# Kernel tuning notes

Hardware: AMD Instinct MI355X
Metric: run time of the kernel (lower is better)

The kernel has to match this reference:

```python
import jax, jax.numpy as jnp
import numpy as np

D_MODEL = 1024
NUM_EXPERTS = 16
TOP_K = 2
TOP_C = 4  # min(M, max(4, 2*K))
RANK = 64  # max(4, d_model // 16) per choose_lowrank_r
TAU = 1.0


def setup_inputs() -> dict:
    key = jax.random.key(0)
    ks = jax.random.split(key, 7)
    B = 32768
    x = jax.random.normal(ks[0], (B, D_MODEL), dtype=jnp.float32)
    # shared encoder Linear(d, d) with bias
    We = jax.random.normal(ks[1], (D_MODEL, D_MODEL), dtype=jnp.float32) / np.sqrt(D_MODEL)
    be = jnp.zeros((D_MODEL,), dtype=jnp.float32)
    # gating Linear(d, M), no bias
    Wg = jax.random.normal(ks[2], (NUM_EXPERTS, D_MODEL), dtype=jnp.float32) / np.sqrt(D_MODEL)
    # per-expert LoRA weights: U: [M, r, d], V: [M, d, r], gamma: [M]
    U = jax.random.normal(ks[3], (NUM_EXPERTS, RANK, D_MODEL), dtype=jnp.float32) / np.sqrt(D_MODEL)
    V = jax.random.normal(ks[4], (NUM_EXPERTS, D_MODEL, RANK), dtype=jnp.float32) / np.sqrt(RANK)
    gamma = jnp.ones((NUM_EXPERTS,), dtype=jnp.float32)
    return {"x": x, "We": We, "be": be, "Wg": Wg, "U": U, "V": V, "gamma": gamma}


def reference(x, We, be, Wg, U, V, gamma):
    B = x.shape[0]
    encoded = x @ We.T + be                       # [B, d]
    logits = (encoded @ Wg.T) / TAU               # [B, M]
    # Top-C candidate selection, then Top-K among candidates
    topc_vals, topc_idx = jax.lax.top_k(logits, TOP_C)          # [B, C]
    topk_vals, pos_in_c = jax.lax.top_k(topc_vals, TOP_K)       # [B, K]
    topk_idx = jnp.take_along_axis(topc_idx, pos_in_c, axis=1)  # [B, K]
    # masked stable softmax over selected logits (matches _stable_masked_softmax)
    e = jnp.exp(topk_vals - jnp.max(topk_vals, axis=1, keepdims=True))
    w = e / (jnp.sum(e, axis=1, keepdims=True) + 1e-12)
    w = jnp.where(w > 1e-12, w, 0.0)  # keep_mask: drop negligible weights
    # scatter routing weights into dense [B, M] combine matrix
    w_full = jnp.zeros((B, NUM_EXPERTS), x.dtype).at[
        jnp.arange(B)[:, None], topk_idx].add(w)
    # expert residual delta: E(x) = x + gamma * V @ silu(U @ x)
    hidden = jax.nn.silu(jnp.einsum('bd,mrd->bmr', encoded, U))  # [B, M, r]
    delta = jnp.einsum('bmr,mdr,bm->bd', hidden, V, w_full * gamma[None, :])
    # y = encoded + sum_k w_k * (E_k(encoded) - encoded); sum_k w_k = 1
    return encoded + delta
```

## Files before the change

kernel.cpp:

```cpp
#include <hip/hip_runtime.h>
#include <stdint.h>

#define B_TOK 32768
#define DM 1024
#define NEXP 16
#define RK 64
#define NPAIR 256
#define TPT 64
#define HT 128
#define GRID_CMB 3072
#define GRID_HID 544
#define MAXTILE 1024

typedef unsigned short u16;
typedef __bf16 bf16x8 __attribute__((ext_vector_type(8)));
typedef float f32x4 __attribute__((ext_vector_type(4)));

__device__ __forceinline__ u16 f2bf(float f) {
  union { float f; uint32_t u; } v; v.f = f;
  return (u16)((v.u + 0x7fffu + ((v.u >> 16) & 1u)) >> 16);
}
__device__ __forceinline__ float bf2f(u16 u) {
  union { uint32_t i; float f; } v; v.i = ((uint32_t)u) << 16; return v.f;
}

__device__ __forceinline__ void gload_lds16(const void* g, void* l) {
  __builtin_amdgcn_global_load_lds(
      (const __attribute__((address_space(1))) void*)g,
      (__attribute__((address_space(3))) void*)l, 16, 0, 0);
}

__global__ void k_prep(const float* __restrict__ s0, u16* __restrict__ d0,
                       const float* __restrict__ s1, u16* __restrict__ d1,
                       const float* __restrict__ s2, u16* __restrict__ d2,
                       const float* __restrict__ Wg, const float* __restrict__ We,
                       double* __restrict__ Wpart) {
  const int b = blockIdx.x;
  if (b < 768) {
    const int seg = b >> 8;
    const int bid = b & 255;
    const float* src = (seg == 0) ? s0 : (seg == 1) ? s1 : s2;
    u16* dst = (seg == 0) ? d0 : (seg == 1) ? d1 : d2;
    int i = bid * 256 + threadIdx.x;
    #pragma unroll
    for (int v = 0; v < 4; ++v) {
      int idx = i + v * 65536;
      float4 f = reinterpret_cast<const float4*>(src)[idx];
      ushort4 o;
      o.x = f2bf(f.x); o.y = f2bf(f.y); o.z = f2bf(f.z); o.w = f2bf(f.w);
      reinterpret_cast<ushort4*>(dst)[idx] = o;
    }
  } else {
    const int pb = b - 768;
    const int kc = pb >> 6;
    const int rem = pb & 63;
    const int e = rem >> 2;
    const int bx = rem & 3;
    const int d = bx * 256 + threadIdx.x;
    const int kbase = kc * 256;
    double a0 = 0.0, a1 = 0.0, a2 = 0.0, a3 = 0.0;
    for (int k = 0; k < 256; k += 4) {
      int kk = kbase + k;
      a0 += (double)Wg[e * DM + kk]     * (double)We[(size_t)kk * DM + d];
      a1 += (double)Wg[e * DM + kk + 1] * (double)We[(size_t)(kk + 1) * DM + d];
      a2 += (double)Wg[e * DM + kk + 2] * (double)We[(size_t)(kk + 2) * DM + d];
      a3 += (double)Wg[e * DM + kk + 3] * (double)We[(size_t)(kk + 3) * DM + d];
    }
    Wpart[((size_t)kc * NEXP + e) * DM + d] = (a0 + a1) + (a2 + a3);
  }
}

__global__ void k_wgred(const double* __restrict__ Wpart, const float* __restrict__ Wg,
                        const float* __restrict__ be,
                        float* __restrict__ Wgeff, float* __restrict__ gbias) {
  const int e = blockIdx.y;
  const int d = blockIdx.x * 256 + threadIdx.x;
  double s = 0.0;
  #pragma unroll
  for (int kc = 0; kc < 4; ++kc)
    s += Wpart[((size_t)kc * NEXP + e) * DM + d];
  Wgeff[e * DM + d] = (float)s;
  if (blockIdx.x == 0 && threadIdx.x == 0) {
    double g = 0.0;
    for (int k = 0; k < DM; ++k) g += (double)be[k] * (double)Wg[e * DM + k];
    gbias[e] = (float)g;
  }
}

#define GT 64
#define GD 128

__global__ __launch_bounds__(256) void k_gating(
    const float* __restrict__ x, u16* __restrict__ x_bf,
    const float* __restrict__ Wgeff, const float* __restrict__ gbias,
    const float* __restrict__ gamma,
    int* __restrict__ tk_pid, float* __restrict__ tk_w0, float* __restrict__ tk_w1,
    int* __restrict__ counts_p, int* __restrict__ counts_e) {
  __shared__ float xs[GT][GD + 4];
  __shared__ float wsd[NEXP][GD + 4];
  __shared__ float lg[GT][NEXP + 2];
  __shared__ int bcnt[NPAIR];
  __shared__ int bexp[NEXP];
  const int tid = threadIdx.x;
  const int tok0 = blockIdx.x * GT;
  const int t0 = (tid >> 3) * 2;
  const int e0 = (tid & 7) * 2;
  bcnt[tid] = 0;
  if (tid < NEXP) bexp[tid] = 0;

  double acc00 = 0.0, acc01 = 0.0, acc10 = 0.0, acc11 = 0.0;

  for (int c = 0; c < DM; c += GD) {
    __syncthreads();
    #pragma unroll
    for (int v = 0; v < (GT * GD / 4) / 256; ++v) {
      int idx = tid + v * 256;
      int r = idx >> 5, cc = idx & 31;
      float4 v4 = *reinterpret_cast<const float4*>(x + (size_t)(tok0 + r) * DM + c + cc * 4);
      *reinterpret_cast<float4*>(&xs[r][cc * 4]) = v4;
      ushort4 o;
      o.x = f2bf(v4.x); o.y = f2bf(v4.y); o.z = f2bf(v4.z); o.w = f2bf(v4.w);
      *reinterpret_cast<ushort4*>(x_bf + (size_t)(tok0 + r) * DM + c + cc * 4) = o;
    }
    #pragma unroll
    for (int v = 0; v < (NEXP * GD / 4) / 256; ++v) {
      int idx = tid + v * 256;
      int r = idx >> 5, cc = idx & 31;
      *reinterpret_cast<float4*>(&wsd[r][cc * 4]) =
          *reinterpret_cast<const float4*>(Wgeff + (size_t)r * DM + c + cc * 4);
    }
    __syncthreads();
    #pragma unroll 8
    for (int d = 0; d < GD; d += 4) {
      float4 xa = *reinterpret_cast<const float4*>(&xs[t0][d]);
      float4 xb = *reinterpret_cast<const float4*>(&xs[t0 + 1][d]);
      float4 wa = *reinterpret_cast<const float4*>(&wsd[e0][d]);
      float4 wb = *reinterpret_cast<const float4*>(&wsd[e0 + 1][d]);
      acc00 += (double)xa.x * wa.x + (double)xa.y * wa.y + (double)xa.z * wa.z + (double)xa.w * wa.w;
      acc01 += (double)xa.x * wb.x + (double)xa.y * wb.y + (double)xa.z * wb.z + (double)xa.w * wb.w;
      acc10 += (double)xb.x * wa.x + (double)xb.y * wa.y + (double)xb.z * wa.z + (double)xb.w * wa.w;
      acc11 += (double)xb.x * wb.x + (double)xb.y * wb.y + (double)xb.z * wb.z + (double)xb.w * wb.w;
    }
  }

  lg[t0][e0]         = (float)(acc00 + (double)gbias[e0]);
  lg[t0][e0 + 1]     = (float)(acc01 + (double)gbias[e0 + 1]);
  lg[t0 + 1][e0]     = (float)(acc10 + (double)gbias[e0]);
  lg[t0 + 1][e0 + 1] = (float)(acc11 + (double)gbias[e0 + 1]);
  __syncthreads();

  if (tid < GT) {
    int tok = tok0 + tid;
    float v0 = lg[tid][0]; int i0 = 0;
    #pragma unroll
    for (int j = 1; j < NEXP; ++j)
      if (lg[tid][j] > v0) { v0 = lg[tid][j]; i0 = j; }
    float v1 = -3.4e38f; int i1 = 0;
    #pragma unroll
    for (int j = 0; j < NEXP; ++j) {
      if (j == i0) continue;
      if (lg[tid][j] > v1) { v1 = lg[tid][j]; i1 = j; }
    }
    float e1 = expf(v1 - v0);
    float denom = 1.0f + e1 + 1e-12f;
    float w0 = 1.0f / denom, w1 = e1 / denom;
    if (!(w0 > 1e-12f)) w0 = 0.0f;
    if (!(w1 > 1e-12f)) w1 = 0.0f;
    int pid = i0 * 16 + i1;
    tk_pid[tok] = pid;
    tk_w0[tok] = w0 * gamma[i0];
    tk_w1[tok] = w1 * gamma[i1];
    atomicAdd(&bcnt[pid], 1);
    atomicAdd(&bexp[i0], 1);
    atomicAdd(&bexp[i1], 1);
  }
  __syncthreads();
  if (bcnt[tid] > 0) atomicAdd(&counts_p[tid], bcnt[tid]);
  if (tid < NEXP && bexp[tid] > 0) atomicAdd(&counts_e[tid], bexp[tid]);
}

__global__ __launch_bounds__(NPAIR) void k_scan(
    const int* __restrict__ counts_p, const int* __restrict__ counts_e,
    int* __restrict__ offs_p, int* __restrict__ curs_p,
    int* __restrict__ offs_e, int* __restrict__ curs_e,
    int* __restrict__ tp_pair, int* __restrict__ tp_loc, int* __restrict__ n_tp,
    int* __restrict__ th_exp, int* __restrict__ th_loc, int* __restrict__ n_th) {
  __shared__ int sc[NPAIR], st[NPAIR];
  __shared__ int seb[NEXP + 1], thb[NEXP + 1];
  const int tid = threadIdx.x;
  const int c = counts_p[tid];
  const int nt = (c + TPT - 1) / TPT;
  sc[tid] = c; st[tid] = nt;
  __syncthreads();
  for (int s = 1; s < NPAIR; s <<= 1) {
    int vc = 0, vt = 0;
    if (tid >= s) { vc = sc[tid - s]; vt = st[tid - s]; }
    __syncthreads();
    sc[tid] += vc; st[tid] += vt;
    __syncthreads();
  }
  const int offc = sc[tid] - c;
  const int offt = st[tid] - nt;
  offs_p[tid] = offc;
  curs_p[tid] = offc;
  if (tid == NPAIR - 1) { offs_p[NPAIR] = sc[tid]; n_tp[0] = st[tid]; }
  for (int q = 0; q < nt; ++q) { tp_pair[offt + q] = tid; tp_loc[offt + q] = q * TPT; }

  if (tid == 0) {
    int s = 0, s2 = 0;
    for (int e = 0; e < NEXP; ++e) {
      seb[e] = s; thb[e] = s2;
      int ce = counts_e[e];
      s += ce; s2 += (ce + HT - 1) / HT;
    }
    seb[NEXP] = s; thb[NEXP] = s2;
    n_th[0] = s2;
  }
  __syncthreads();
  if (tid <= NEXP) offs_e[tid] = seb[tid];
  if (tid < NEXP) {
    curs_e[tid] = seb[tid];
    int ce = counts_e[tid];
    int ntt = (ce + HT - 1) / HT;
    for (int q = 0; q < ntt; ++q) { th_exp[thb[tid] + q] = tid; th_loc[thb[tid] + q] = q * HT; }
  }
}

__global__ __launch_bounds__(256) void k_scatter(
    const int* __restrict__ tk_pid, const float* __restrict__ tk_w0,
    const float* __restrict__ tk_w1,
    int* __restrict__ curs_p, int* __restrict__ curs_e,
    int* __restrict__ a_tok, int* __restrict__ a_h0,
    int* __restrict__ a_h1,
    int* __restrict__ e_tok, float* __restrict__ e_w) {
  __shared__ int hp[NPAIR];
  __shared__ int he[NEXP];
  __shared__ int bp[NPAIR];
  __shared__ int beB[NEXP];
  const int tid = threadIdx.x;
  const int tok = blockIdx.x * 256 + tid;
  hp[tid] = 0;
  if (tid < NEXP) he[tid] = 0;
  __syncthreads();

  const int pid = tk_pid[tok];
  const int i0 = pid >> 4, i1 = pid & 15;
  const int rp = atomicAdd(&hp[pid], 1);
  const int r0 = atomicAdd(&he[i0], 1);
  const int r1 = atomicAdd(&he[i1], 1);
  __syncthreads();

  if (hp[tid] > 0) bp[tid] = atomicAdd(&curs_p[tid], hp[tid]);
  if (tid < NEXP && he[tid] > 0) beB[tid] = atomicAdd(&curs_e[tid], he[tid]);
  __syncthreads();

  const int posp = bp[pid] + rp;
  const int pos0 = beB[i0] + r0;
  const int pos1 = beB[i1] + r1;
  a_tok[posp] = tok;
  a_h0[posp] = pos0;
  a_h1[posp] = pos1;
  e_tok[pos0] = tok; e_w[pos0] = tk_w0[tok];
  e_tok[pos1] = tok; e_w[pos1] = tk_w1[tok];
}

__global__ __launch_bounds__(256) void k_encoder(
    const u16* __restrict__ A, const u16* __restrict__ Bm,
    const float* __restrict__ bias, u16* __restrict__ Cb) {
  __shared__ __align__(16) u16 As0[128 * 64];
  __shared__ __align__(16) u16 Bs0[128 * 64];
  __shared__ __align__(16) u16 As1[128 * 64];
  __shared__ __align__(16) u16 Bs1[128 * 64];
  const int nwg = gridDim.x * gridDim.y;
  const int orig = blockIdx.y * gridDim.x + blockIdx.x;
  const int qq = nwg >> 3;
  const int swz = (orig & 7) * qq + (orig >> 3);
  const int m0 = (swz / gridDim.x) * 128, n0 = (swz % gridDim.x) * 128;
  const int tid = threadIdx.x;
  const int lane = tid & 63, wave = tid >> 6;
  const int wr = wave >> 1, wc = wave & 1;
  const int lrow = lane & 15, lhi = lane >> 4;

  f32x4 acc[4][4];
  #pragma unroll
  for (int i = 0; i < 4; ++i)
    #pragma unroll
    for (int j = 0; j < 4; ++j) acc[i][j] = (f32x4){0.f, 0.f, 0.f, 0.f};

  const u16* gA0; const u16* gA1; const u16* gA2; const u16* gA3;
  const u16* gB0; const u16* gB1; const u16* gB2; const u16* gB3;
  int dOf0, dOf1, dOf2, dOf3;
  {
    int slot, row, c, sc;
    slot = tid;         row = slot >> 3; c = slot & 7; sc = (c ^ (row & 7)) * 8;
    gA0 = A + (size_t)(m0 + row) * DM + sc; gB0 = Bm + (size_t)(n0 + row) * DM + sc; dOf0 = slot * 8;
    slot = tid + 256;   row = slot >> 3; c = slot & 7; sc = (c ^ (row & 7)) * 8;
    gA1 = A + (size_t)(m0 + row) * DM + sc; gB1 = Bm + (size_t)(n0 + row) * DM + sc; dOf1 = slot * 8;
    slot = tid + 512;   row = slot >> 3; c = slot & 7; sc = (c ^ (row & 7)) * 8;
    gA2 = A + (size_t)(m0 + row) * DM + sc; gB2 = Bm + (size_t)(n0 + row) * DM + sc; dOf2 = slot * 8;
    slot = tid + 768;   row = slot >> 3; c = slot & 7; sc = (c ^ (row & 7)) * 8;
    gA3 = A + (size_t)(m0 + row) * DM + sc; gB3 = Bm + (size_t)(n0 + row) * DM + sc; dOf3 = slot * 8;
  }

  const int rk0 = ((0 + lhi) ^ (lrow & 7)) * 8;
  const int rk1 = ((4 + lhi) ^ (lrow & 7)) * 8;

  auto STAGE = [&](u16* Ad, u16* Bd, int k0) {
    gload_lds16(gA0 + k0, Ad + dOf0);
    gload_lds16(gA1 + k0, Ad + dOf1);
    gload_lds16(gA2 + k0, Ad + dOf2);
    gload_lds16(gA3 + k0, Ad + dOf3);
    gload_lds16(gB0 + k0, Bd + dOf0);
    gload_lds16(gB1 + k0, Bd + dOf1);
    gload_lds16(gB2 + k0, Bd + dOf2);
    gload_lds16(gB3 + k0, Bd + dOf3);
  };
  auto COMPUTE = [&](const u16* Ar, const u16* Br) {
    #pragma unroll
    for (int kk = 0; kk < 2; ++kk) {
      const int rk = kk ? rk1 : rk0;
      bf16x8 a[4], b[4];
      #pragma unroll
      for (int mi = 0; mi < 4; ++mi)
        a[mi] = *reinterpret_cast<const bf16x8*>(&Ar[(wr * 64 + mi * 16 + lrow) * 64 + rk]);
      #pragma unroll
      for (int nj = 0; nj < 4; ++nj)
        b[nj] = *reinterpret_cast<const bf16x8*>(&Br[(wc * 64 + nj * 16 + lrow) * 64 + rk]);
      #pragma unroll
      for (int mi = 0; mi < 4; ++mi)
        #pragma unroll
        for (int nj = 0; nj < 4; ++nj)
          acc[mi][nj] = __builtin_amdgcn_mfma_f32_16x16x32_bf16(a[mi], b[nj], acc[mi][nj], 0, 0, 0);
    }
  };

  STAGE(As0, Bs0, 0);
  #pragma unroll
  for (int i = 0; i < 8; ++i) {
    STAGE(As1, Bs1, i * 128 + 64);
    asm volatile("s_waitcnt vmcnt(8)" ::: "memory");
    __builtin_amdgcn_s_barrier();
    COMPUTE(As0, Bs0);
    __builtin_amdgcn_s_barrier();
    if (i < 7) {
      STAGE(As0, Bs0, i * 128 + 128);
      asm volatile("s_waitcnt vmcnt(8)" ::: "memory");
    } else {
      asm volatile("s_waitcnt vmcnt(0)" ::: "memory");
    }
    __builtin_amdgcn_s_barrier();
    COMPUTE(As1, Bs1);
    __builtin_amdgcn_s_barrier();
  }

  const int orow = lhi * 4, ocol = lrow;
  #pragma unroll
  for (int mi = 0; mi < 4; ++mi) {
    #pragma unroll
    for (int nj = 0; nj < 4; ++nj) {
      int gcol = n0 + wc * 64 + nj * 16 + ocol;
      float bv = bias[gcol];
      #pragma unroll
      for (int r = 0; r < 4; ++r) {
        int grow = m0 + wr * 64 + mi * 16 + orow + r;
        Cb[(size_t)grow * DM + gcol] = f2bf(acc[mi][nj][r] + bv);
      }
    }
  }
}

__global__ __launch_bounds__(256) void k_hidden(
    const u16* __restrict__ Enc, const u16* __restrict__ Ub,
    const int* __restrict__ offs_e, const int* __restrict__ th_exp,
    const int* __restrict__ th_loc, const int* __restrict__ n_th,
    const int* __restrict__ e_tok, const float* __restrict__ e_w,
    u16* __restrict__ Hws) {
  const int bswz = (blockIdx.x & 7) * (GRID_HID >> 3) + (blockIdx.x >> 3);
  if (bswz >= n_th[0]) return;
  const int e = th_exp[bswz];
  const int loc0 = th_loc[bswz];
  const int base = offs_e[e];
  const int cnt = offs_e[e + 1] - base;
  const int tid = threadIdx.x;
  const int lane = tid & 63, wave = tid >> 6;
  const int lrow = lane & 15;
  const int lkb = (lane >> 4) * 16;

  __shared__ float s_ew[HT];
  __shared__ __align__(16) u16 Us[64 * 512];
  if (tid < HT) {
    int i = loc0 + tid;
    s_ew[tid] = (i < cnt) ? e_w[base + i] : 0.0f;
  }

  const u16* aP[2];
  #pragma unroll
  for (int mi = 0; mi < 2; ++mi) {
    int ridx = loc0 + wave * 32 + mi * 16 + lrow;
    int v = ridx < cnt;
    int tok = e_tok[base + (v ? ridx : 0)];
    aP[mi] = Enc + (size_t)tok * DM + (lane >> 4) * 8;
  }

  f32x4 acc[2][4];
  #pragma unroll
  for (int i = 0; i < 2; ++i)
    #pragma unroll
    for (int j = 0; j < 4; ++j) acc[i][j] = (f32x4){0.f, 0.f, 0.f, 0.f};

  const char* Ue = (const char*)(Ub + (size_t)e * RK * DM);

  for (int half = 0; half < 2; ++half) {
    __syncthreads();
    #pragma unroll
    for (int it = 0; it < 16; ++it) {
      int D = (tid + it * 256) * 16;
      int row = D >> 10, bo = D & 1023;
      int sbo = bo ^ ((row & 7) << 4);
      gload_lds16(Ue + (size_t)row * 2048 + half * 1024 + sbo, ((char*)Us) + D);
    }
    __syncthreads();
    #pragma unroll 4
    for (int step = 0; step < 16; ++step) {
      const int k0 = half * 512 + step * 32;
      bf16x8 b[4];
      #pragma unroll
      for (int nj = 0; nj < 4; ++nj) {
        int n = nj * 16 + lrow;
        int bofs = n * 1024 + ((step * 64 + lkb) ^ ((n & 7) << 4));
        b[nj] = *reinterpret_cast<const bf16x8*>(((const char*)Us) + bofs);
      }
      bf16x8 a0 = *reinterpret_cast<const bf16x8*>(aP[0] + k0);
      bf16x8 a1 = *reinterpret_cast<const bf16x8*>(aP[1] + k0);
      #pragma unroll
      for (int nj = 0; nj < 4; ++nj) {
        acc[0][nj] = __builtin_amdgcn_mfma_f32_16x16x32_bf16(a0, b[nj], acc[0][nj], 0, 0, 0);
        acc[1][nj] = __builtin_amdgcn_mfma_f32_16x16x32_bf16(a1, b[nj], acc[1][nj], 0, 0, 0);
      }
    }
  }

  #pragma unroll
  for (int mi = 0; mi < 2; ++mi)
    #pragma unroll
    for (int nj = 0; nj < 4; ++nj)
      #pragma unroll
      for (int rr = 0; rr < 4; ++rr) {
        int rloc = wave * 32 + mi * 16 + (lane >> 4) * 4 + rr;
        if (loc0 + rloc < cnt) {
          float z = acc[mi][nj][rr];
          float h = z / (1.0f + expf(-z)) * s_ew[rloc];
          Hws[(size_t)(base + loc0 + rloc) * RK + nj * 16 + (lane & 15)] = f2bf(h);
        }
      }
}

__global__ __launch_bounds__(256) void k_combine(
    const u16* __restrict__ Enc, const u16* __restrict__ Vb,
    const u16* __restrict__ Hws, const int* __restrict__ offs_p,
    const int* __restrict__ tp_pair, const int* __restrict__ tp_loc,
    const int* __restrict__ n_tp, const int* __restrict__ a_tok,
    const int* __restrict__ a_h0, const int* __restrict__ a_h1,
    float* __restrict__ Out) {
  const int bswz = (blockIdx.x & 7) * (GRID_CMB >> 3) + (blockIdx.x >> 3);
  const int t = bswz >> 2;
  const int p = bswz & 3;
  if (t >= n_tp[0]) return;
  const int pid = tp_pair[t];
  const int pe0 = pid >> 4, pe1 = pid & 15;
  const int base = offs_p[pid];
  const int cnt = offs_p[pid + 1] - base;
  const int loc0 = tp_loc[t];
  const int tid = threadIdx.x;
  const int lane = tid & 63, wave = tid >> 6;

  __shared__ int s_tok[TPT];
  __shared__ int s_h0[TPT];
  __shared__ int s_h1[TPT];
  __shared__ int s_val[TPT];
  if (tid < TPT) {
    int idx = loc0 + tid;
    int v = idx < cnt;
    int pp = base + (v ? idx : 0);
    s_val[tid] = v;
    s_tok[tid] = a_tok[pp];
    s_h0[tid] = a_h0[pp];
    s_h1[tid] = a_h1[pp];
  }
  __syncthreads();

  const int lrow = lane & 15, lk = (lane >> 4) * 8;
  const int col0 = p * 256 + wave * 64;

  bf16x8 hb[4][4];
  #pragma unroll
  for (int kk = 0; kk < 4; ++kk)
    #pragma unroll
    for (int tf = 0; tf < 4; ++tf) {
      int tok = tf * 16 + lrow;
      int hidx = (kk < 2) ? s_h0[tok] : s_h1[tok];
      hb[kk][tf] = *reinterpret_cast<const bf16x8*>(
          Hws + (size_t)hidx * RK + (kk & 1) * 32 + lk);
    }

  ushort4 encv[4][4];
  #pragma unroll
  for (int mi = 0; mi < 4; ++mi)
    #pragma unroll
    for (int tf = 0; tf < 4; ++tf) {
      int tok = tf * 16 + (lane & 15);
      int d = col0 + mi * 16 + (lane >> 4) * 4;
      encv[mi][tf] = *reinterpret_cast<const ushort4*>(Enc + (size_t)s_tok[tok] * DM + d);
    }

  const u16* V0 = Vb + (size_t)pe0 * DM * RK;
  const u16* V1 = Vb + (size_t)pe1 * DM * RK;

  f32x4 acc2[4][4];
  #pragma unroll
  for (int i = 0; i < 4; ++i)
    #pragma unroll
    for (int j = 0; j < 4; ++j) acc2[i][j] = (f32x4){0.f, 0.f, 0.f, 0.f};

  #pragma unroll
  for (int kk = 0; kk < 4; ++kk) {
    const u16* Vsel = (kk < 2) ? V0 : V1;
    const int kof = (kk & 1) * 32 + lk;
    #pragma unroll
    for (int mi = 0; mi < 4; ++mi) {
      int d = col0 + mi * 16 + lrow;
      bf16x8 va = *reinterpret_cast<const bf16x8*>(Vsel + (size_t)d * RK + kof);
      #pragma unroll
      for (int tf = 0; tf < 4; ++tf)
        acc2[mi][tf] = __builtin_amdgcn_mfma_f32_16x16x32_bf16(va, hb[kk][tf], acc2[mi][tf], 0, 0, 0);
    }
  }

  #pragma unroll
  for (int mi = 0; mi < 4; ++mi)
    #pragma unroll
    for (int tf = 0; tf < 4; ++tf) {
      int tok = tf * 16 + (lane & 15);
      if (!s_val[tok]) continue;
      int d = col0 + mi * 16 + (lane >> 4) * 4;
      size_t ro = (size_t)s_tok[tok] * DM + d;
      ushort4 ev = encv[mi][tf];
      float4 o;
      o.x = acc2[mi][tf][0] + bf2f(ev.x);
      o.y = acc2[mi][tf][1] + bf2f(ev.y);
      o.z = acc2[mi][tf][2] + bf2f(ev.z);
      o.w = acc2[mi][tf][3] + bf2f(ev.w);
      *reinterpret_cast<float4*>(Out + ro) = o;
    }
}

extern "C" void kernel_launch(void* const* d_in, const int* in_sizes, int n_in,
                              void* d_out, int out_size, void* d_ws, size_t ws_size,
                              hipStream_t stream) {
  const float* x = (const float*)d_in[0];
  const float* We = (const float*)d_in[1];
  const float* be = (const float*)d_in[2];
  const float* Wg = (const float*)d_in[3];
  const float* U = (const float*)d_in[4];
  const float* V = (const float*)d_in[5];
  const float* gamma = (const float*)d_in[6];
  float* Out = (float*)d_out;

  char* ws = (char*)d_ws;
  size_t off = 0;
  auto alloc = [&](size_t bytes) -> void* {
    void* p = ws + off;
    off += (bytes + 255) & ~(size_t)255;
    return p;
  };
  u16* x_bf   = (u16*)alloc((size_t)B_TOK * DM * 2);
  u16* enc_bf = (u16*)alloc((size_t)B_TOK * DM * 2);
  u16* We_bf  = (u16*)alloc((size_t)DM * DM * 2);
  u16* U_bf   = (u16*)alloc((size_t)NEXP * RK * DM * 2);
  u16* V_bf   = (u16*)alloc((size_t)NEXP * DM * RK * 2);
  u16* Hws    = (u16*)alloc(((size_t)2 * B_TOK + HT) * RK * 2);
  double* Wpart = (double*)alloc((size_t)4 * NEXP * DM * 8);
  float* Wgeff = (float*)alloc((size_t)NEXP * DM * 4);
  float* gbias = (float*)alloc(NEXP * 4);
  int* tk_pid  = (int*)alloc((size_t)B_TOK * 4);
  float* tk_w0 = (float*)alloc((size_t)B_TOK * 4);
  float* tk_w1 = (float*)alloc((size_t)B_TOK * 4);
  int* counts_p = (int*)alloc(NPAIR * 4);
  int* counts_e = (int*)alloc(NEXP * 4);
  int* offs_p   = (int*)alloc((NPAIR + 1) * 4);
  int* curs_p   = (int*)alloc(NPAIR * 4);
  int* offs_e   = (int*)alloc((NEXP + 1) * 4);
  int* curs_e   = (int*)alloc(NEXP * 4);
  int* tp_pair  = (int*)alloc(MAXTILE * 4);
  int* tp_loc   = (int*)alloc(MAXTILE * 4);
  int* n_tp     = (int*)alloc(256);
  int* th_exp   = (int*)alloc(MAXTILE * 4);
  int* th_loc   = (int*)alloc(MAXTILE * 4);
  int* n_th     = (int*)alloc(256);
  int* a_tok   = (int*)alloc((size_t)B_TOK * 4);
  int* a_h0    = (int*)alloc((size_t)B_TOK * 4);
  int* a_h1    = (int*)alloc((size_t)B_TOK * 4);
  int* e_tok   = (int*)alloc(((size_t)2 * B_TOK + HT) * 4);
  float* e_w   = (float*)alloc(((size_t)2 * B_TOK + HT) * 4);
  (void)ws_size; (void)in_sizes; (void)n_in; (void)out_size;

  hipMemsetAsync(counts_p, 0, NPAIR * 4, stream);
  hipMemsetAsync(counts_e, 0, NEXP * 4, stream);

  k_prep<<<1024, 256, 0, stream>>>(We, We_bf, U, U_bf, V, V_bf, Wg, We, Wpart);
  k_wgred<<<dim3(4, 16), 256, 0, stream>>>(Wpart, Wg, be, Wgeff, gbias);
  k_gating<<<B_TOK / GT, 256, 0, stream>>>(x, x_bf, Wgeff, gbias, gamma,
                                           tk_pid, tk_w0, tk_w1, counts_p, counts_e);
  k_scan<<<1, NPAIR, 0, stream>>>(counts_p, counts_e, offs_p, curs_p, offs_e, curs_e,
                                  tp_pair, tp_loc, n_tp, th_exp, th_loc, n_th);
  k_scatter<<<B_TOK / 256, 256, 0, stream>>>(tk_pid, tk_w0, tk_w1, curs_p, curs_e,
                                             a_tok, a_h0, a_h1, e_tok, e_w);
  k_encoder<<<dim3(DM / 128, B_TOK / 128), 256, 0, stream>>>(x_bf, We_bf, be, enc_bf);
  k_hidden<<<GRID_HID, 256, 0, stream>>>(enc_bf, U_bf, offs_e, th_exp, th_loc, n_th,
                                         e_tok, e_w, Hws);
  k_combine<<<GRID_CMB, 256, 0, stream>>>(enc_bf, V_bf, Hws, offs_p, tp_pair, tp_loc,
                                          n_tp, a_tok, a_h0, a_h1, Out);
}
```

Baseline: 320.9 us.

## Split gating logit reduction over two K halves with separate routing kernel

The gating kernel is split into two parts. The first computes partial fp64 logits over half of the model dimension per block, which doubles the grid to 1024 blocks. A new routing kernel then sums the partials, adds the bias, and does the top-2 selection, softmax and counting. The aim is more parallelism in the fp64-heavy gating dot products, at the cost of one extra launch and an 8 MB round trip for the partial logits.

```diff
diff --git a/kernel.cpp b/kernel.cpp
--- a/kernel.cpp
+++ b/kernel.cpp
@@ -90,27 +90,22 @@
 #define GT 64
 #define GD 128
 
-__global__ __launch_bounds__(256) void k_gating(
+__global__ __launch_bounds__(256) void k_gath(
     const float* __restrict__ x, u16* __restrict__ x_bf,
-    const float* __restrict__ Wgeff, const float* __restrict__ gbias,
-    const float* __restrict__ gamma,
-    int* __restrict__ tk_pid, float* __restrict__ tk_w0, float* __restrict__ tk_w1,
-    int* __restrict__ counts_p, int* __restrict__ counts_e) {
+    const float* __restrict__ Wgeff,
+    double* __restrict__ Lpart) {
   __shared__ float xs[GT][GD + 4];
   __shared__ float wsd[NEXP][GD + 4];
-  __shared__ float lg[GT][NEXP + 2];
-  __shared__ int bcnt[NPAIR];
-  __shared__ int bexp[NEXP];
   const int tid = threadIdx.x;
   const int tok0 = blockIdx.x * GT;
+  const int kc = blockIdx.y;
+  const int cbase = kc * 512;
   const int t0 = (tid >> 3) * 2;
   const int e0 = (tid & 7) * 2;
-  bcnt[tid] = 0;
-  if (tid < NEXP) bexp[tid] = 0;
 
   double acc00 = 0.0, acc01 = 0.0, acc10 = 0.0, acc11 = 0.0;
 
-  for (int c = 0; c < DM; c += GD) {
+  for (int c = cbase; c < cbase + 512; c += GD) {
     __syncthreads();
     #pragma unroll
     for (int v = 0; v < (GT * GD / 4) / 256; ++v) {
@@ -143,37 +138,55 @@
     }
   }
 
-  lg[t0][e0]         = (float)(acc00 + (double)gbias[e0]);
-  lg[t0][e0 + 1]     = (float)(acc01 + (double)gbias[e0 + 1]);
-  lg[t0 + 1][e0]     = (float)(acc10 + (double)gbias[e0]);
-  lg[t0 + 1][e0 + 1] = (float)(acc11 + (double)gbias[e0 + 1]);
-  __syncthreads();
-
-  if (tid < GT) {
-    int tok = tok0 + tid;
-    float v0 = lg[tid][0]; int i0 = 0;
-    #pragma unroll
-    for (int j = 1; j < NEXP; ++j)
-      if (lg[tid][j] > v0) { v0 = lg[tid][j]; i0 = j; }
-    float v1 = -3.4e38f; int i1 = 0;
-    #pragma unroll
-    for (int j = 0; j < NEXP; ++j) {
-      if (j == i0) continue;
-      if (lg[tid][j] > v1) { v1 = lg[tid][j]; i1 = j; }
-    }
-    float e1 = expf(v1 - v0);
-    float denom = 1.0f + e1 + 1e-12f;
-    float w0 = 1.0f / denom, w1 = e1 / denom;
-    if (!(w0 > 1e-12f)) w0 = 0.0f;
-    if (!(w1 > 1e-12f)) w1 = 0.0f;
-    int pid = i0 * 16 + i1;
-    tk_pid[tok] = pid;
-    tk_w0[tok] = w0 * gamma[i0];
-    tk_w1[tok] = w1 * gamma[i1];
-    atomicAdd(&bcnt[pid], 1);
-    atomicAdd(&bexp[i0], 1);
-    atomicAdd(&bexp[i1], 1);
-  }
+  double* Lp = Lpart + ((size_t)kc * B_TOK) * NEXP;
+  Lp[(size_t)(tok0 + t0) * NEXP + e0]           = acc00;
+  Lp[(size_t)(tok0 + t0) * NEXP + e0 + 1]       = acc01;
+  Lp[(size_t)(tok0 + t0 + 1) * NEXP + e0]       = acc10;
+  Lp[(size_t)(tok0 + t0 + 1) * NEXP + e0 + 1]   = acc11;
+}
+
+__global__ __launch_bounds__(256) void k_route(
+    const double* __restrict__ Lpart, const float* __restrict__ gbias,
+    const float* __restrict__ gamma,
+    int* __restrict__ tk_pid, float* __restrict__ tk_w0, float* __restrict__ tk_w1,
+    int* __restrict__ counts_p, int* __restrict__ counts_e) {
+  __shared__ int bcnt[NPAIR];
+  __shared__ int bexp[NEXP];
+  const int tid = threadIdx.x;
+  const int tok = blockIdx.x * 256 + tid;
+  bcnt[tid] = 0;
+  if (tid < NEXP) bexp[tid] = 0;
+  __syncthreads();
+
+  const double* L0 = Lpart + (size_t)tok * NEXP;
+  const double* L1 = Lpart + ((size_t)B_TOK + tok) * NEXP;
+  float lg[NEXP];
+  #pragma unroll
+  for (int j = 0; j < NEXP; ++j)
+    lg[j] = (float)(L0[j] + L1[j] + (double)gbias[j]);
+
+  float v0 = lg[0]; int i0 = 0;
+  #pragma unroll
+  for (int j = 1; j < NEXP; ++j)
+    if (lg[j] > v0) { v0 = lg[j]; i0 = j; }
+  float v1 = -3.4e38f; int i1 = 0;
+  #pragma unroll
+  for (int j = 0; j < NEXP; ++j) {
+    if (j == i0) continue;
+    if (lg[j] > v1) { v1 = lg[j]; i1 = j; }
+  }
+  float e1 = expf(v1 - v0);
+  float denom = 1.0f + e1 + 1e-12f;
+  float w0 = 1.0f / denom, w1 = e1 / denom;
+  if (!(w0 > 1e-12f)) w0 = 0.0f;
+  if (!(w1 > 1e-12f)) w1 = 0.0f;
+  int pid = i0 * 16 + i1;
+  tk_pid[tok] = pid;
+  tk_w0[tok] = w0 * gamma[i0];
+  tk_w1[tok] = w1 * gamma[i1];
+  atomicAdd(&bcnt[pid], 1);
+  atomicAdd(&bexp[i0], 1);
+  atomicAdd(&bexp[i1], 1);
   __syncthreads();
   if (bcnt[tid] > 0) atomicAdd(&counts_p[tid], bcnt[tid]);
   if (tid < NEXP && bexp[tid] > 0) atomicAdd(&counts_e[tid], bexp[tid]);
@@ -580,6 +593,7 @@
   u16* V_bf   = (u16*)alloc((size_t)NEXP * DM * RK * 2);
   u16* Hws    = (u16*)alloc(((size_t)2 * B_TOK + HT) * RK * 2);
   double* Wpart = (double*)alloc((size_t)4 * NEXP * DM * 8);
+  double* Lpart = (double*)alloc((size_t)2 * B_TOK * NEXP * 8);
   float* Wgeff = (float*)alloc((size_t)NEXP * DM * 4);
   float* gbias = (float*)alloc(NEXP * 4);
   int* tk_pid  = (int*)alloc((size_t)B_TOK * 4);
@@ -609,7 +623,8 @@
 
   k_prep<<<1024, 256, 0, stream>>>(We, We_bf, U, U_bf, V, V_bf, Wg, We, Wpart);
   k_wgred<<<dim3(4, 16), 256, 0, stream>>>(Wpart, Wg, be, Wgeff, gbias);
-  k_gating<<<B_TOK / GT, 256, 0, stream>>>(x, x_bf, Wgeff, gbias, gamma,
+  k_gath<<<dim3(B_TOK / GT, 2), 256, 0, stream>>>(x, x_bf, Wgeff, Lpart);
+  k_route<<<B_TOK / 256, 256, 0, stream>>>(Lpart, gbias, gamma,
                                            tk_pid, tk_w0, tk_w1, counts_p, counts_e);
   k_scan<<<1, NPAIR, 0, stream>>>(counts_p, counts_e, offs_p, curs_p, offs_e, curs_e,
                                   tp_pair, tp_loc, n_tp, th_exp, th_loc, n_th);
```

Measured after the change: 329.7 us. +2.7%, slower.
